# Performance work log

Hardware: AMD Instinct MI355X
Metric: run time of the kernel (lower is better)

## Reference

```python
import jax, jax.numpy as jnp
import numpy as np

DIM = 4096
N_HEADS = 32
N_KV = 8
HD = 128
SW = 4096          # sliding window / cache length
B = 32             # max_batch_size (decode batch)
MAX_SEQ = 8192
START_POS = 4000
CURRENT_POS = 4000

def _nearest_32(n):
    return ((n + 31) // 32) * 32

PADDED_LEN = min(_nearest_32(START_POS + 1), SW)  # 4032

def _rope_tables():
    inv_freq = 1.0 / (10000.0 ** (np.arange(0, HD, 2, dtype=np.float32) / HD))
    t = np.arange(MAX_SEQ, dtype=np.float32)
    freqs = np.outer(t, inv_freq)                       # [MAX_SEQ, HD/2]
    emb = np.concatenate([freqs, freqs], axis=-1)       # [MAX_SEQ, HD]
    return jnp.asarray(np.cos(emb)), jnp.asarray(np.sin(emb))

def rotate_half(u):
    u1, u2 = jnp.split(u, 2, axis=-1)
    return jnp.concatenate([-u2, u1], axis=-1)

def setup_inputs() -> dict:
    key = jax.random.key(0)
    ks = jax.random.split(key, 6)
    cos_cached, sin_cached = _rope_tables()
    return {
        "x": jax.random.normal(ks[0], (1, 1, B, DIM), jnp.float32),
        "wqkv": jax.random.normal(ks[1], (DIM, DIM + 2 * N_KV * HD), jnp.float32) * 0.02,
        "wo": jax.random.normal(ks[2], (DIM, DIM), jnp.float32) * 0.02,
        "cache_k": jax.random.normal(ks[3], (B, N_KV, SW, HD), jnp.float32) * 0.5,
        "cache_v": jax.random.normal(ks[4], (B, N_KV, SW, HD), jnp.float32) * 0.5,
        "cos_cached": cos_cached,
        "sin_cached": sin_cached,
        "attn_mask": jnp.zeros((B, N_HEADS, 1, PADDED_LEN), jnp.float32),
        "start_pos": START_POS,
        "current_pos": CURRENT_POS,
    }

def reference(x, wqkv, wo, cache_k, cache_v, cos_cached, sin_cached, attn_mask,
              start_pos, current_pos):
    group = N_HEADS // N_KV
    padded_len = min(_nearest_32(start_pos + 1), SW)
    scale = 1.0 / jnp.sqrt(jnp.float32(HD))

    # fused QKV projection: x (1,1,B,DIM) @ wqkv -> (B, DIM + 2*N_KV*HD)
    xqkv = x[0, 0] @ wqkv
    q = xqkv[:, :DIM].reshape(B, N_HEADS, HD)
    k = xqkv[:, DIM:DIM + N_KV * HD].reshape(B, N_KV, HD)
    v = xqkv[:, DIM + N_KV * HD:].reshape(B, N_KV, HD)

    # rotary embedding at position start_pos (single decode token)
    cos = cos_cached[start_pos]   # [HD]
    sin = sin_cached[start_pos]
    q = q * cos + rotate_half(q) * sin
    k = k * cos + rotate_half(k) * sin

    # sliding-window KV cache update at current_pos
    cache_k = cache_k.at[:, :, current_pos, :].set(k)
    cache_v = cache_v.at[:, :, current_pos, :].set(v)
    keys = cache_k[:, :, :padded_len, :]     # [B, N_KV, L, HD]
    values = cache_v[:, :, :padded_len, :]

    # grouped attention: q heads grouped by kv head
    qg = q.reshape(B, N_KV, group, HD)
    scores = jnp.einsum('bkgd,bkld->bkgl', qg, keys) * scale
    scores = scores + attn_mask.reshape(B, N_KV, group, padded_len)
    probs = jax.nn.softmax(scores, axis=-1)
    out = jnp.einsum('bkgl,bkld->bkgd', probs, values)   # [B, N_KV, group, HD]

    # concat heads and output projection
    dense = out.reshape(B, DIM) @ wo
    return dense.reshape(1, 1, B, DIM)
```

## Files before the change

### kernel.cpp

```cpp
#include <hip/hip_runtime.h>
#include <hip/hip_bf16.h>

typedef unsigned int u32;
typedef unsigned short u16;

__device__ __forceinline__ u16 f2bf(float f){ u32 x; __builtin_memcpy(&x,&f,4); u32 r=(x+0x7fffu+((x>>16)&1u))>>16; return (u16)r; }
__device__ __forceinline__ float lo2f(u32 u){ u32 x=u<<16; float f; __builtin_memcpy(&f,&x,4); return f; }
__device__ __forceinline__ float hi2f(u32 u){ u32 x=u&0xffff0000u; float f; __builtin_memcpy(&f,&x,4); return f; }

__global__ __launch_bounds__(256) void transpose_x(
    const float* __restrict__ x, float* __restrict__ xt)
{
    __shared__ float ld[32][65];
    const int t = threadIdx.x;
    const int g = blockIdx.x;
    #pragma unroll
    for (int i=0;i<8;++i) {
        const int e = i*256 + t;
        const int b = e >> 6, dd = e & 63;
        ld[b][dd] = x[(size_t)b*4096 + g*64 + dd];
    }
    __syncthreads();
    #pragma unroll
    for (int i=0;i<8;++i) {
        const int e = i*256 + t;
        const int dd = e >> 5, b = e & 31;
        xt[(size_t)(g*64 + dd)*32 + b] = ld[b][dd];
    }
}

__global__ __launch_bounds__(256) void gemm_splitk_t(
    const float* __restrict__ At, const float2* __restrict__ W2,
    float* __restrict__ P, int K, int N, int dps)
{
    const int j2 = blockIdx.x*256 + threadIdx.x;
    const int s = blockIdx.y;
    float acc0[32], acc1[32];
    #pragma unroll
    for (int b=0;b<32;++b){ acc0[b]=0.f; acc1[b]=0.f; }
    const int d0 = s*dps, d1 = d0 + dps;
    const int halfN = N >> 1;
    #pragma unroll 2
    for (int d=d0; d<d1; ++d) {
        const float2 wv = W2[(size_t)d*halfN + j2];
        const float* __restrict__ Ad = At + d*32;
        #pragma unroll
        for (int b=0;b<32;++b) {
            const float av = Ad[b];
            acc0[b] = fmaf(av, wv.x, acc0[b]);
            acc1[b] = fmaf(av, wv.y, acc1[b]);
        }
    }
    float* Pp = P + (size_t)(s*32)*N + 2*j2;
    #pragma unroll
    for (int b=0;b<32;++b)
        *reinterpret_cast<float2*>(Pp + (size_t)b*N) = make_float2(acc0[b], acc1[b]);
}

__global__ __launch_bounds__(256) void qkv_finish(
    const float* __restrict__ P, const float* __restrict__ cosc,
    const float* __restrict__ sinc, const int* __restrict__ spp,
    float* __restrict__ qws, float* __restrict__ kn, float* __restrict__ vn,
    int splits)
{
    __shared__ float sh[256];
    const int t = threadIdx.x;
    const int col = blockIdx.x*256 + t;
    const int b = blockIdx.y;
    float v = 0.f;
    for (int s=0;s<splits;++s) v += P[(size_t)(s*32+b)*6144 + col];
    sh[t] = v;
    __syncthreads();
    if (col < 5120) {
        const int d = col & 127;
        const int pt = (t & ~127) | ((d<64)? d+64 : d-64);
        const float pv = sh[pt];
        const int spos = *spp;
        const float c  = cosc[spos*128 + d];
        const float sn = sinc[spos*128 + d];
        const float rot = (d<64)? -pv : pv;
        const float val = fmaf(v, c, rot*sn);
        if (col < 4096) qws[(size_t)b*4096 + col] = val;
        else            kn[(size_t)b*1024 + (col-4096)] = val;
    } else {
        vn[(size_t)b*1024 + (col-5120)] = v;
    }
}

__global__ __launch_bounds__(1024, 4) void attn_kernel(
    const float* __restrict__ qws, const float* __restrict__ Kc,
    const float* __restrict__ Vc, const float* __restrict__ kn,
    const float* __restrict__ vn, const float* __restrict__ mask,
    const int* __restrict__ curp, float* __restrict__ aout_t,
    const int PL, const int SW)
{
    __shared__ float scoresS[4*4100];
    __shared__ uint2 probsP[4096];
    __shared__ float obuf[16][4][128];
    __shared__ float redm[16][4];
    __shared__ float reds[16][4];

    const int t = threadIdx.x;
    const int lane = t & 63;
    const int w = t >> 6;
    const int b  = blockIdx.x >> 3;
    const int kv = blockIdx.x & 7;
    const int cur = *curp;

    const size_t mat = (size_t)(b*8+kv);
    const float* __restrict__ Kb  = Kc + mat*(size_t)SW*128;
    const float* __restrict__ knr = kn + mat*128;
    const float* __restrict__ qbase = qws + (size_t)(b*32 + kv*4)*128;

    const int l   = lane & 15;
    const int grp = lane >> 4;
    float qv[4][8];
    #pragma unroll
    for (int h=0;h<4;++h)
        #pragma unroll
        for (int j=0;j<8;++j)
            qv[h][j] = qbase[h*128 + l*8 + j];

    const int rpw = PL >> 4;
    const int rb0 = w * rpw;
    for (int g=0; g<rpw; g+=4) {
        const int r = rb0 + g + grp;
        const float* __restrict__ row = (r==cur) ? knr : (Kb + (size_t)r*128);
        const float4 ka = *reinterpret_cast<const float4*>(row + l*8);
        const float4 kb4 = *reinterpret_cast<const float4*>(row + l*8 + 4);
        float kf[8];
        kf[0]=ka.x; kf[1]=ka.y; kf[2]=ka.z; kf[3]=ka.w;
        kf[4]=kb4.x; kf[5]=kb4.y; kf[6]=kb4.z; kf[7]=kb4.w;
        float sc0=0.f, sc1=0.f, sc2=0.f, sc3=0.f;
        #pragma unroll
        for (int j=0;j<8;++j) {
            sc0 = fmaf(qv[0][j], kf[j], sc0);
            sc1 = fmaf(qv[1][j], kf[j], sc1);
            sc2 = fmaf(qv[2][j], kf[j], sc2);
            sc3 = fmaf(qv[3][j], kf[j], sc3);
        }
        #pragma unroll
        for (int off=8; off; off>>=1) {
            sc0 += __shfl_xor(sc0, off, 16);
            sc1 += __shfl_xor(sc1, off, 16);
            sc2 += __shfl_xor(sc2, off, 16);
            sc3 += __shfl_xor(sc3, off, 16);
        }
        if (l < 4) {
            const float v = (l==0)?sc0:(l==1)?sc1:(l==2)?sc2:sc3;
            scoresS[l*4100 + r] = v;
        }
    }
    __syncthreads();

    const float scale = 0.08838834764831845f;
    const size_t mbase = ((size_t)b*32 + (size_t)kv*4)*(size_t)PL;
    float s[4][4];
    #pragma unroll
    for (int i=0;i<4;++i) {
        const int p = i*1024 + t;
        if (p < PL) {
            #pragma unroll
            for (int h=0;h<4;++h) {
                const float mv = mask[mbase + (size_t)h*PL + p];
                s[h][i] = fmaf(scoresS[h*4100 + p], scale, mv);
            }
        } else {
            #pragma unroll
            for (int h=0;h<4;++h) s[h][i] = -3.0e38f;
        }
    }

    float lm[4];
    #pragma unroll
    for (int h=0;h<4;++h)
        lm[h] = fmaxf(fmaxf(s[h][0],s[h][1]), fmaxf(s[h][2],s[h][3]));
    #pragma unroll
    for (int off=1; off<64; off<<=1) {
        #pragma unroll
        for (int h=0;h<4;++h) lm[h] = fmaxf(lm[h], __shfl_xor(lm[h], off, 64));
    }
    if (lane==0) {
        #pragma unroll
        for (int h=0;h<4;++h) redm[w][h] = lm[h];
    }
    __syncthreads();
    float M[4];
    #pragma unroll
    for (int h=0;h<4;++h) {
        float m = redm[0][h];
        #pragma unroll
        for (int ww=1;ww<16;++ww) m = fmaxf(m, redm[ww][h]);
        M[h] = m;
    }

    float ls[4] = {0.f,0.f,0.f,0.f};
    #pragma unroll
    for (int i=0;i<4;++i) {
        #pragma unroll
        for (int h=0;h<4;++h) {
            const float e = __expf(s[h][i] - M[h]);
            s[h][i] = e;
            ls[h] += e;
        }
    }
    #pragma unroll
    for (int off=1; off<64; off<<=1) {
        #pragma unroll
        for (int h=0;h<4;++h) ls[h] += __shfl_xor(ls[h], off, 64);
    }
    if (lane==0) {
        #pragma unroll
        for (int h=0;h<4;++h) reds[w][h] = ls[h];
    }
    __syncthreads();
    float inv[4];
    #pragma unroll
    for (int h=0;h<4;++h) {
        float sm = reds[0][h];
        #pragma unroll
        for (int ww=1;ww<16;++ww) sm += reds[ww][h];
        inv[h] = 1.f / sm;
    }

    #pragma unroll
    for (int i=0;i<4;++i) {
        const int p = i*1024 + t;
        if (p < PL) {
            const u32 plo = (u32)f2bf(s[0][i]*inv[0]) | ((u32)f2bf(s[1][i]*inv[1]) << 16);
            const u32 phi = (u32)f2bf(s[2][i]*inv[2]) | ((u32)f2bf(s[3][i]*inv[3]) << 16);
            probsP[p] = make_uint2(plo, phi);
        }
    }
    __syncthreads();

    const float* __restrict__ Vb  = Vc + mat*(size_t)SW*128;
    const float* __restrict__ vnr = vn + mat*128;
    const int chunk = PL >> 4;
    const int p0 = w*chunk, p1 = p0 + chunk;
    float a0[4] = {0.f,0.f,0.f,0.f}, a1[4] = {0.f,0.f,0.f,0.f};
    #pragma unroll 8
    for (int p=p0; p<p1; ++p) {
        const float* row = (p==cur) ? vnr : (Vb + (size_t)p*128);
        const float2 vv = *reinterpret_cast<const float2*>(row + 2*lane);
        const uint2 pp = probsP[p];
        const float pr0 = lo2f(pp.x), pr1 = hi2f(pp.x);
        const float pr2 = lo2f(pp.y), pr3 = hi2f(pp.y);
        a0[0]=fmaf(pr0,vv.x,a0[0]); a1[0]=fmaf(pr0,vv.y,a1[0]);
        a0[1]=fmaf(pr1,vv.x,a0[1]); a1[1]=fmaf(pr1,vv.y,a1[1]);
        a0[2]=fmaf(pr2,vv.x,a0[2]); a1[2]=fmaf(pr2,vv.y,a1[2]);
        a0[3]=fmaf(pr3,vv.x,a0[3]); a1[3]=fmaf(pr3,vv.y,a1[3]);
    }
    #pragma unroll
    for (int h=0;h<4;++h)
        *reinterpret_cast<float2*>(&obuf[w][h][2*lane]) = make_float2(a0[h], a1[h]);
    __syncthreads();

    if (t < 512) {
        const int h = t >> 7;
        const int d = t & 127;
        float sum = obuf[0][h][d];
        #pragma unroll
        for (int ww=1;ww<16;++ww) sum += obuf[ww][h][d];
        const int col = (kv*4 + h)*128 + d;
        aout_t[(size_t)col*32 + b] = sum;
    }
}

__global__ __launch_bounds__(256) void wo_finish(
    const float* __restrict__ P, float* __restrict__ out, int splits)
{
    const int col = blockIdx.x*256 + threadIdx.x;
    const int b = blockIdx.y;
    float v = 0.f;
    for (int s=0;s<splits;++s) v += P[(size_t)(s*32+b)*4096 + col];
    out[(size_t)b*4096 + col] = v;
}

extern "C" void kernel_launch(void* const* d_in, const int* in_sizes, int n_in,
                              void* d_out, int out_size, void* d_ws, size_t ws_size,
                              hipStream_t stream)
{
    const float* x    = (const float*)d_in[0];
    const float* wqkv = (const float*)d_in[1];
    const float* wo   = (const float*)d_in[2];
    const float* cK   = (const float*)d_in[3];
    const float* cV   = (const float*)d_in[4];
    const float* cosc = (const float*)d_in[5];
    const float* sinc = (const float*)d_in[6];
    const float* mask = (const float*)d_in[7];
    const int* sp   = (const int*)d_in[8];
    const int* cp   = (const int*)d_in[9];

    const int PL = in_sizes[7] / (32*32);
    const int SW = in_sizes[3] / (32*8*128);

    char* ws = (char*)d_ws;
    float* xt    = (float*)(ws);
    float* qws   = (float*)(ws + 524288);
    float* aout_t= (float*)(ws + 2*524288);
    float* kn    = (float*)(ws + 3*524288);
    float* vn    = (float*)(ws + 3*524288 + 131072);
    float* Pbuf  = (float*)(ws + 3*524288 + 2*131072);

    const int splits = 32;
    const int dps = 4096 / splits;

    transpose_x<<<64, 256, 0, stream>>>(x, xt);
    gemm_splitk_t<<<dim3(12, splits), 256, 0, stream>>>(xt, (const float2*)wqkv, Pbuf, 4096, 6144, dps);
    qkv_finish<<<dim3(24, 32), 256, 0, stream>>>(Pbuf, cosc, sinc, sp, qws, kn, vn, splits);

    attn_kernel<<<256, 1024, 0, stream>>>(qws, cK, cV, kn, vn, mask, cp, aout_t, PL, SW);

    gemm_splitk_t<<<dim3(8, splits), 256, 0, stream>>>(aout_t, (const float2*)wo, Pbuf, 4096, 4096, dps);
    wo_finish<<<dim3(16, 32), 256, 0, stream>>>(Pbuf, (float*)d_out, splits);
}
```

Before: 310.7 us.

## Fuse softmax into PV loop with online softmax; double split-K factor

Replaces the separate block-wide softmax (two reductions, two barriers, bf16 probability buffer in shared memory) with an online-softmax update fused into each wave's P·V loop. Each wave keeps running max and sum per head, and the partial results are rescaled and merged at the end. The cost is that every lane in a wave now recomputes the same exps and mask loads for every row, adding redundant work. Separately, the split-K count for the projection GEMMs goes from 32 to 64, giving more parallelism but a larger partial buffer and more work in the finish kernels.

After: 329.8 us. 1.06x slower.

```diff
diff --git a/kernel.cpp b/kernel.cpp
--- a/kernel.cpp
+++ b/kernel.cpp
@@ -95,7 +95,6 @@
     const int PL, const int SW)
 {
     __shared__ float scoresS[4*4100];
-    __shared__ uint2 probsP[4096];
     __shared__ float obuf[16][4][128];
     __shared__ float redm[16][4];
     __shared__ float reds[16][4];
@@ -155,101 +154,44 @@
 
     const float scale = 0.08838834764831845f;
     const size_t mbase = ((size_t)b*32 + (size_t)kv*4)*(size_t)PL;
-    float s[4][4];
-    #pragma unroll
-    for (int i=0;i<4;++i) {
-        const int p = i*1024 + t;
-        if (p < PL) {
-            #pragma unroll
-            for (int h=0;h<4;++h) {
-                const float mv = mask[mbase + (size_t)h*PL + p];
-                s[h][i] = fmaf(scoresS[h*4100 + p], scale, mv);
-            }
-        } else {
-            #pragma unroll
-            for (int h=0;h<4;++h) s[h][i] = -3.0e38f;
-        }
-    }
-
-    float lm[4];
-    #pragma unroll
-    for (int h=0;h<4;++h)
-        lm[h] = fmaxf(fmaxf(s[h][0],s[h][1]), fmaxf(s[h][2],s[h][3]));
-    #pragma unroll
-    for (int off=1; off<64; off<<=1) {
-        #pragma unroll
-        for (int h=0;h<4;++h) lm[h] = fmaxf(lm[h], __shfl_xor(lm[h], off, 64));
-    }
-    if (lane==0) {
-        #pragma unroll
-        for (int h=0;h<4;++h) redm[w][h] = lm[h];
-    }
-    __syncthreads();
-    float M[4];
-    #pragma unroll
-    for (int h=0;h<4;++h) {
-        float m = redm[0][h];
-        #pragma unroll
-        for (int ww=1;ww<16;++ww) m = fmaxf(m, redm[ww][h]);
-        M[h] = m;
-    }
-
-    float ls[4] = {0.f,0.f,0.f,0.f};
-    #pragma unroll
-    for (int i=0;i<4;++i) {
-        #pragma unroll
-        for (int h=0;h<4;++h) {
-            const float e = __expf(s[h][i] - M[h]);
-            s[h][i] = e;
-            ls[h] += e;
-        }
-    }
-    #pragma unroll
-    for (int off=1; off<64; off<<=1) {
-        #pragma unroll
-        for (int h=0;h<4;++h) ls[h] += __shfl_xor(ls[h], off, 64);
-    }
-    if (lane==0) {
-        #pragma unroll
-        for (int h=0;h<4;++h) reds[w][h] = ls[h];
-    }
-    __syncthreads();
-    float inv[4];
-    #pragma unroll
-    for (int h=0;h<4;++h) {
-        float sm = reds[0][h];
-        #pragma unroll
-        for (int ww=1;ww<16;++ww) sm += reds[ww][h];
-        inv[h] = 1.f / sm;
-    }
-
-    #pragma unroll
-    for (int i=0;i<4;++i) {
-        const int p = i*1024 + t;
-        if (p < PL) {
-            const u32 plo = (u32)f2bf(s[0][i]*inv[0]) | ((u32)f2bf(s[1][i]*inv[1]) << 16);
-            const u32 phi = (u32)f2bf(s[2][i]*inv[2]) | ((u32)f2bf(s[3][i]*inv[3]) << 16);
-            probsP[p] = make_uint2(plo, phi);
-        }
-    }
-    __syncthreads();
-
     const float* __restrict__ Vb  = Vc + mat*(size_t)SW*128;
     const float* __restrict__ vnr = vn + mat*128;
     const int chunk = PL >> 4;
     const int p0 = w*chunk, p1 = p0 + chunk;
+
+    float m0=-3.0e38f, m1=-3.0e38f, m2=-3.0e38f, m3=-3.0e38f;
+    float l0=0.f, l1=0.f, l2=0.f, l3=0.f;
     float a0[4] = {0.f,0.f,0.f,0.f}, a1[4] = {0.f,0.f,0.f,0.f};
-    #pragma unroll 8
+
+    #pragma unroll 4
     for (int p=p0; p<p1; ++p) {
         const float* row = (p==cur) ? vnr : (Vb + (size_t)p*128);
         const float2 vv = *reinterpret_cast<const float2*>(row + 2*lane);
-        const uint2 pp = probsP[p];
-        const float pr0 = lo2f(pp.x), pr1 = hi2f(pp.x);
-        const float pr2 = lo2f(pp.y), pr3 = hi2f(pp.y);
-        a0[0]=fmaf(pr0,vv.x,a0[0]); a1[0]=fmaf(pr0,vv.y,a1[0]);
-        a0[1]=fmaf(pr1,vv.x,a0[1]); a1[1]=fmaf(pr1,vv.y,a1[1]);
-        a0[2]=fmaf(pr2,vv.x,a0[2]); a1[2]=fmaf(pr2,vv.y,a1[2]);
-        a0[3]=fmaf(pr3,vv.x,a0[3]); a1[3]=fmaf(pr3,vv.y,a1[3]);
+
+        const float sc0 = fmaf(scoresS[         p], scale, mask[mbase              + p]);
+        const float sc1 = fmaf(scoresS[ 4100 +  p], scale, mask[mbase +   (size_t)PL + p]);
+        const float sc2 = fmaf(scoresS[ 8200 +  p], scale, mask[mbase + 2*(size_t)PL + p]);
+        const float sc3 = fmaf(scoresS[12300 +  p], scale, mask[mbase + 3*(size_t)PL + p]);
+
+        const float n0 = fmaxf(m0, sc0), n1 = fmaxf(m1, sc1);
+        const float n2 = fmaxf(m2, sc2), n3 = fmaxf(m3, sc3);
+        const float f0 = __expf(m0 - n0), f1 = __expf(m1 - n1);
+        const float f2 = __expf(m2 - n2), f3 = __expf(m3 - n3);
+        const float e0 = __expf(sc0 - n0), e1 = __expf(sc1 - n1);
+        const float e2 = __expf(sc2 - n2), e3 = __expf(sc3 - n3);
+        m0 = n0; m1 = n1; m2 = n2; m3 = n3;
+        l0 = fmaf(l0, f0, e0); l1 = fmaf(l1, f1, e1);
+        l2 = fmaf(l2, f2, e2); l3 = fmaf(l3, f3, e3);
+
+        a0[0] = fmaf(e0, vv.x, a0[0]*f0); a1[0] = fmaf(e0, vv.y, a1[0]*f0);
+        a0[1] = fmaf(e1, vv.x, a0[1]*f1); a1[1] = fmaf(e1, vv.y, a1[1]*f1);
+        a0[2] = fmaf(e2, vv.x, a0[2]*f2); a1[2] = fmaf(e2, vv.y, a1[2]*f2);
+        a0[3] = fmaf(e3, vv.x, a0[3]*f3); a1[3] = fmaf(e3, vv.y, a1[3]*f3);
+    }
+
+    if (lane==0) {
+        redm[w][0]=m0; redm[w][1]=m1; redm[w][2]=m2; redm[w][3]=m3;
+        reds[w][0]=l0; reds[w][1]=l1; reds[w][2]=l2; reds[w][3]=l3;
     }
     #pragma unroll
     for (int h=0;h<4;++h)
@@ -259,11 +201,18 @@
     if (t < 512) {
         const int h = t >> 7;
         const int d = t & 127;
-        float sum = obuf[0][h][d];
-        #pragma unroll
-        for (int ww=1;ww<16;++ww) sum += obuf[ww][h][d];
+        float M = redm[0][h];
+        #pragma unroll
+        for (int ww=1;ww<16;++ww) M = fmaxf(M, redm[ww][h]);
+        float num = 0.f, den = 0.f;
+        #pragma unroll
+        for (int ww=0;ww<16;++ww) {
+            const float f = __expf(redm[ww][h] - M);
+            num = fmaf(f, obuf[ww][h][d], num);
+            den = fmaf(f, reds[ww][h], den);
+        }
         const int col = (kv*4 + h)*128 + d;
-        aout_t[(size_t)col*32 + b] = sum;
+        aout_t[(size_t)col*32 + b] = num/den;
     }
 }
 
@@ -303,7 +252,7 @@
     float* vn    = (float*)(ws + 3*524288 + 131072);
     float* Pbuf  = (float*)(ws + 3*524288 + 2*131072);
 
-    const int splits = 32;
+    const int splits = 64;
     const int dps = 4096 / splits;
 
     transpose_x<<<64, 256, 0, stream>>>(x, xt);
```
